# Optimization experiments

Hardware: AMD Instinct MI355X
Metric: run time of the kernel (lower is better)

The kernel has to match this reference:

```python
import jax, jax.numpy as jnp
import numpy as np

DIM = 384
HEADS = 12
WS = 7


def setup_inputs() -> dict:
    key = jax.random.key(0)
    ks = jax.random.split(key, 5)
    B, H, W = 16, 56, 56
    x = jax.random.normal(ks[0], (B, H * W, DIM), dtype=jnp.float32)
    # torch Linear weight (out,in) used as x @ W here, qkv_bias=False
    w_qkv = jax.random.normal(ks[1], (DIM, 3 * DIM), dtype=jnp.float32) * 0.02
    w_proj = jax.random.normal(ks[2], (DIM, DIM), dtype=jnp.float32) * 0.02
    b_proj = jax.random.normal(ks[3], (DIM,), dtype=jnp.float32) * 0.02
    # depthwise 3x3 conv (groups=dim): HWIO kernel (3,3,1,DIM), bias=True
    w_conv = jax.random.normal(ks[4], (3, 3, 1, DIM), dtype=jnp.float32) * 0.02
    b_conv = jnp.zeros((DIM,), jnp.float32)
    return {"x": x, "w_qkv": w_qkv, "w_proj": w_proj, "b_proj": b_proj,
            "w_conv": w_conv, "b_conv": b_conv, "H": H, "W": W}


def reference(x, w_qkv, w_proj, b_proj, w_conv, b_conv, H, W):
    B, N, C = x.shape
    hd = C // HEADS
    scale = hd ** (-0.5)
    hg, wg = H // WS, W // WS  # H,W chosen divisible by ws (no-pad fast path)

    qkv = x @ w_qkv  # (B, N, 3C)
    q, k, v = jnp.split(qkv, 3, axis=-1)

    def to_win(t):
        # (B,N,C) -> (B, n_windows, heads, ws*ws, head_dim)
        t = t.reshape(B, hg, WS, wg, WS, HEADS, hd)
        return t.transpose(0, 1, 3, 5, 2, 4, 6).reshape(B, hg * wg, HEADS, WS * WS, hd)

    qw, kw, vw = to_win(q), to_win(k), to_win(v)

    attn = jax.nn.softmax(jnp.einsum('bwhqd,bwhkd->bwhqk', qw, kw) * scale, axis=-1)
    out = jnp.einsum('bwhqk,bwhkd->bwhqd', attn, vw)
    # merge windows back: (B,nw,heads,q,d) -> (B,N,C)
    out = out.reshape(B, hg, wg, HEADS, WS, WS, hd)
    out = out.transpose(0, 1, 4, 2, 5, 3, 6).reshape(B, N, C)

    # LIM: win2img(img2win(v)) is just v as (B,C,H,W); depthwise 3x3 conv
    v_img = v.reshape(B, H, W, C).transpose(0, 3, 1, 2)
    v_lim = jax.lax.conv_general_dilated(
        v_img, w_conv, window_strides=(1, 1), padding='SAME',
        dimension_numbers=('NCHW', 'HWIO', 'NCHW'), feature_group_count=C)
    v_lim = v_lim + b_conv[None, :, None, None]
    v_lim = v_lim.reshape(B, C, N).transpose(0, 2, 1)  # (B, N, C)

    out = out + v_lim
    return out @ w_proj + b_proj
```

## Files before the change

### kernel.cpp

```cpp
#include <hip/hip_runtime.h>
#include <cstdint>
#include <cstddef>

typedef __bf16 bf16x8 __attribute__((ext_vector_type(8)));
typedef float floatx4 __attribute__((ext_vector_type(4)));

#define DEV static __device__ __forceinline__

DEV float bf2f(uint16_t u) {
    union { uint32_t i; float f; } x; x.i = ((uint32_t)u) << 16; return x.f;
}
DEV uint16_t f2bf(float f) {
    uint32_t u = __float_as_uint(f);
    uint32_t r = (u + 0x7FFFu + ((u >> 16) & 1u)) >> 16;
    return (uint16_t)r;
}
DEV bf16x8 as_bf8(uint4 u) {
    union { uint4 u; bf16x8 b; } c; c.u = u; return c.b;
}
DEV void g2l16(const void* g, void* l) {
    __builtin_amdgcn_global_load_lds(
        (const __attribute__((address_space(1))) void*)g,
        (__attribute__((address_space(3))) void*)l, 16, 0, 0);
}

union U16x8 { uint16_t h[8]; uint4 u; };

constexpr int DIMC  = 384;
constexpr int HEADS = 12;
constexpr int IMH   = 56, IMW = 56;
constexpr int NTOK  = IMH * IMW;
constexpr int BATCH = 16;
constexpr int MTOT  = BATCH * NTOK;
constexpr int QKVLD = 3 * DIMC;
constexpr int GK    = 384;
constexpr int MTILES_PAD = 200;

constexpr int CVTB  = (MTOT * DIMC) / (8 * 256);
constexpr int TQKVB = (GK * QKVLD) / 256;
constexpr int TPRJB = (GK * DIMC) / 256;

__global__ __launch_bounds__(256) void prep_kernel(
    const float* __restrict__ x,      uint16_t* __restrict__ xb,
    const float* __restrict__ w_qkv,  uint16_t* __restrict__ wqkvT,
    const float* __restrict__ w_proj, uint16_t* __restrict__ wprojT)
{
    int bid = blockIdx.x;
    int t   = threadIdx.x;
    if (bid < CVTB) {
        size_t i = ((size_t)bid * 256 + t) * 8;
        float4 a = *(const float4*)(x + i);
        float4 b = *(const float4*)(x + i + 4);
        U16x8 o;
        o.h[0] = f2bf(a.x); o.h[1] = f2bf(a.y); o.h[2] = f2bf(a.z); o.h[3] = f2bf(a.w);
        o.h[4] = f2bf(b.x); o.h[5] = f2bf(b.y); o.h[6] = f2bf(b.z); o.h[7] = f2bf(b.w);
        *(uint4*)(xb + i) = o.u;
    } else if (bid < CVTB + TQKVB) {
        int idx = (bid - CVTB) * 256 + t;
        int r = idx % GK, c = idx / GK;
        wqkvT[idx] = f2bf(w_qkv[(size_t)r * QKVLD + c]);
    } else {
        int idx = (bid - CVTB - TQKVB) * 256 + t;
        int r = idx % GK, c = idx / GK;
        wprojT[idx] = f2bf(w_proj[(size_t)r * DIMC + c]);
    }
}

template<bool CF32>
__global__ __launch_bounds__(512) void gemm_bt(const uint16_t* __restrict__ A,
                                               const uint16_t* __restrict__ Bt,
                                               const float* __restrict__ bias,
                                               void* __restrict__ Cptr,
                                               int N)
{
    __shared__ __align__(16) uint16_t sA[2][256 * 32];
    __shared__ __align__(16) uint16_t sB[2][128 * 32];

    const int t    = threadIdx.x;
    const int NB   = N >> 7;
    const int bid  = blockIdx.x;
    const int chunk = bid / (8 * NB);
    const int r     = bid % (8 * NB);
    const int bm    = chunk * 8 + (r & 7);
    const int bn    = r >> 3;
    const int wave = t >> 6, lane = t & 63;
    const int wm   = (wave >> 1) * 64;
    const int wn   = (wave & 1) * 64;
    const int lr   = lane & 15, quad = lane >> 4;
    const bool mvalid = (bm * 256 + 256) <= MTOT;

    const uint16_t* Ag = A  + (size_t)(bm * 256 + (t >> 2)) * GK + (t & 3) * 8;
    const uint16_t* Bg = Bt + (size_t)(bn * 128 + (t >> 2)) * GK + (t & 3) * 8;

    auto stage = [&](int buf, int k0) {
        g2l16(Ag + k0, sA[buf] + wave * 512);
        g2l16(Ag + (size_t)128 * GK + k0, sA[buf] + 4096 + wave * 512);
        g2l16(Bg + k0, sB[buf] + wave * 512);
    };

    floatx4 acc[4][4] = {};

    stage(0, 0);
    __syncthreads();

    #pragma unroll
    for (int ks = 0; ks < 12; ++ks) {
        const int cur = ks & 1;
        if (ks < 11) stage(cur ^ 1, (ks + 1) * 32);

        bf16x8 af[4], bfr[4];
        #pragma unroll
        for (int mt = 0; mt < 4; ++mt)
            af[mt] = *(const bf16x8*)&sA[cur][(wm + mt * 16 + lr) * 32 + quad * 8];
        #pragma unroll
        for (int nt = 0; nt < 4; ++nt)
            bfr[nt] = *(const bf16x8*)&sB[cur][(wn + nt * 16 + lr) * 32 + quad * 8];
        #pragma unroll
        for (int mt = 0; mt < 4; ++mt)
            #pragma unroll
            for (int nt = 0; nt < 4; ++nt)
                acc[mt][nt] = __builtin_amdgcn_mfma_f32_16x16x32_bf16(
                    af[mt], bfr[nt], acc[mt][nt], 0, 0, 0);

        __syncthreads();
    }

    if (!mvalid) return;

    #pragma unroll
    for (int mt = 0; mt < 4; ++mt) {
        #pragma unroll
        for (int nt = 0; nt < 4; ++nt) {
            int gc = bn * 128 + wn + nt * 16 + lr;
            float bv = bias ? bias[gc] : 0.0f;
            int gr0 = bm * 256 + wm + mt * 16 + quad * 4;
            #pragma unroll
            for (int i = 0; i < 4; ++i) {
                if constexpr (CF32) {
                    ((float*)Cptr)[(size_t)(gr0 + i) * N + gc] = acc[mt][nt][i] + bv;
                } else {
                    ((uint16_t*)Cptr)[(size_t)(gr0 + i) * N + gc] = f2bf(acc[mt][nt][i] + bv);
                }
            }
        }
    }
}

constexpr int PLD = 72;
constexpr int WAVE_ELEMS = 32 * PLD + 81 * 32;

__global__ __launch_bounds__(128) void attn_mfma(const uint16_t* __restrict__ qkv,
                                                 const float* __restrict__ wconv,
                                                 const float* __restrict__ bconv,
                                                 uint16_t* __restrict__ y)
{
    __shared__ uint16_t lds[2][WAVE_ELEMS];
    __shared__ float    warr_all[2][320];

    const int wave = threadIdx.x >> 6;
    const int lane = threadIdx.x & 63;
    const int unit = blockIdx.x * 2 + wave;
    const int h  = unit % HEADS;
    const int w  = (unit / HEADS) & 63;
    const int b  = unit / (HEADS * 64);
    const int wy = w >> 3, wx = w & 7;
    const int lr = lane & 15, quad = lane >> 4;

    uint16_t* Vt    = lds[wave];
    uint16_t* Vhalo = lds[wave] + 32 * PLD;
    float*    warr  = warr_all[wave];

    #pragma unroll
    for (int it = 0; it < 5; ++it) {
        int idx = it * 64 + lane;
        if (idx < 288) warr[idx] = wconv[(idx >> 5) * DIMC + h * 32 + (idx & 31)];
    }
    if (lane < 32) warr[288 + lane] = bconv[h * 32 + lane];

    #pragma unroll
    for (int it = 0; it < 6; ++it) {
        int u = it * 16 + (lane >> 2);
        int g = lane & 3;
        if (u < 81) {
            int hy = u / 9, hx = u % 9;
            int iy = wy * 7 + hy - 1, ix = wx * 7 + hx - 1;
            uint4 val{0, 0, 0, 0};
            if (iy >= 0 && iy < IMH && ix >= 0 && ix < IMW)
                val = *(const uint4*)(qkv + (size_t)(b * NTOK + iy * IMW + ix) * QKVLD
                                      + 2 * DIMC + h * 32 + g * 8);
            *(uint4*)&Vhalo[u * 32 + g * 8] = val;
        }
    }

    auto rowbase = [&](int i, int which) -> const uint16_t* {
        int py = i / 7, px = i % 7;
        int n = (wy * 7 + py) * IMW + wx * 7 + px;
        return qkv + (size_t)(b * NTOK + n) * QKVLD + which * DIMC + h * 32;
    };

    uint4 qf[4], kf[4];
    #pragma unroll
    for (int tm = 0; tm < 4; ++tm) {
        int i = tm * 16 + lr;
        if (i < 49) {
            qf[tm] = *(const uint4*)(rowbase(i, 0) + quad * 8);
            kf[tm] = *(const uint4*)(rowbase(i, 1) + quad * 8);
        } else {
            qf[tm] = uint4{0, 0, 0, 0};
            kf[tm] = uint4{0, 0, 0, 0};
        }
    }

    {
        int j = lane;
        if (j < 49) {
            int hrow = (j / 7 + 1) * 9 + (j % 7 + 1);
            #pragma unroll
            for (int p = 0; p < 4; ++p) {
                U16x8 tmp; tmp.u = *(const uint4*)&Vhalo[hrow * 32 + p * 8];
                #pragma unroll
                for (int q = 0; q < 8; ++q) Vt[(p * 8 + q) * PLD + j] = tmp.h[q];
            }
        } else {
            #pragma unroll
            for (int d = 0; d < 32; ++d) Vt[d * PLD + j] = 0;
        }
    }

    floatx4 S[4][4] = {};
    #pragma unroll
    for (int ta = 0; ta < 4; ++ta)
        #pragma unroll
        for (int tb = 0; tb < 4; ++tb)
            S[ta][tb] = __builtin_amdgcn_mfma_f32_16x16x32_bf16(
                as_bf8(kf[ta]), as_bf8(qf[tb]), S[ta][tb], 0, 0, 0);

    const float scale = 0.17677669529663687f;
    float psum[4] = {0.f, 0.f, 0.f, 0.f};
    #pragma unroll
    for (int ta = 0; ta < 4; ++ta) {
        #pragma unroll
        for (int tb = 0; tb < 4; ++tb) {
            #pragma unroll
            for (int i = 0; i < 4; ++i) {
                float e;
                if (ta < 3) e = __expf(S[ta][tb][i] * scale);
                else        e = (quad == 0 && i == 0)
                                ? __expf(S[ta][tb][i] * scale) : 0.0f;
                S[ta][tb][i] = e;
                psum[tb] += e;
            }
        }
    }
    #pragma unroll
    for (int tb = 0; tb < 4; ++tb) {
        float s = psum[tb];
        s += __shfl_xor(s, 16);
        s += __shfl_xor(s, 32);
        psum[tb] = 1.0f / s;
    }

    uint32_t pkv[4][4][2];
    #pragma unroll
    for (int ta = 0; ta < 4; ++ta) {
        #pragma unroll
        for (int tb = 0; tb < 4; ++tb) {
            #pragma unroll
            for (int hh = 0; hh < 2; ++hh) {
                float lo = S[ta][tb][2 * hh]     * psum[tb];
                float hi = S[ta][tb][2 * hh + 1] * psum[tb];
                asm("v_cvt_pk_bf16_f32 %0, %1, %2"
                    : "=v"(pkv[ta][tb][hh]) : "v"(lo), "v"(hi));
            }
        }
    }

    const int lo_lane = (quad & 1) * 32 + lr;
    const bool hiq = quad >= 2;
    floatx4 Ot[2][4] = {};
    #pragma unroll
    for (int kk = 0; kk < 2; ++kk) {
        uint4 pfr[4];
        #pragma unroll
        for (int tb = 0; tb < 4; ++tb) {
            uint32_t a0 = (uint32_t)__shfl((int)pkv[kk * 2][tb][0],     lo_lane);
            uint32_t b0 = (uint32_t)__shfl((int)pkv[kk * 2 + 1][tb][0], lo_lane);
            uint32_t a1 = (uint32_t)__shfl((int)pkv[kk * 2][tb][1],     lo_lane);
            uint32_t b1 = (uint32_t)__shfl((int)pkv[kk * 2 + 1][tb][1], lo_lane);
            uint32_t a2 = (uint32_t)__shfl((int)pkv[kk * 2][tb][0],     lo_lane + 16);
            uint32_t b2 = (uint32_t)__shfl((int)pkv[kk * 2 + 1][tb][0], lo_lane + 16);
            uint32_t a3 = (uint32_t)__shfl((int)pkv[kk * 2][tb][1],     lo_lane + 16);
            uint32_t b3 = (uint32_t)__shfl((int)pkv[kk * 2 + 1][tb][1], lo_lane + 16);
            pfr[tb] = uint4{hiq ? b0 : a0, hiq ? b1 : a1,
                            hiq ? b2 : a2, hiq ? b3 : a3};
        }
        bf16x8 vf[2];
        #pragma unroll
        for (int td = 0; td < 2; ++td)
            vf[td] = *(const bf16x8*)&Vt[(td * 16 + lr) * PLD + kk * 32 + quad * 8];
        #pragma unroll
        for (int td = 0; td < 2; ++td)
            #pragma unroll
            for (int tb = 0; tb < 4; ++tb)
                Ot[td][tb] = __builtin_amdgcn_mfma_f32_16x16x32_bf16(
                    vf[td], as_bf8(pfr[tb]), Ot[td][tb], 0, 0, 0);
    }

    uint16_t* convb = Vt;
    #pragma unroll
    for (int it = 0; it < 4; ++it) {
        int u = it * 64 + lane;
        if (u < 196) {
            int j = u >> 2, g = u & 3;
            int py = j / 7, px = j % 7;
            float acc[8];
            {
                float4 b0 = *(const float4*)(warr + 288 + g * 8);
                float4 b1 = *(const float4*)(warr + 288 + g * 8 + 4);
                acc[0] = b0.x; acc[1] = b0.y; acc[2] = b0.z; acc[3] = b0.w;
                acc[4] = b1.x; acc[5] = b1.y; acc[6] = b1.z; acc[7] = b1.w;
            }
            #pragma unroll
            for (int ky = 0; ky < 3; ++ky) {
                #pragma unroll
                for (int kx = 0; kx < 3; ++kx) {
                    int hrow = (py + ky) * 9 + (px + kx);
                    U16x8 v; v.u = *(const uint4*)&Vhalo[hrow * 32 + g * 8];
                    const float* wp = warr + (ky * 3 + kx) * 32 + g * 8;
                    float4 w0 = *(const float4*)wp;
                    float4 w1 = *(const float4*)(wp + 4);
                    acc[0] += bf2f(v.h[0]) * w0.x;
                    acc[1] += bf2f(v.h[1]) * w0.y;
                    acc[2] += bf2f(v.h[2]) * w0.z;
                    acc[3] += bf2f(v.h[3]) * w0.w;
                    acc[4] += bf2f(v.h[4]) * w1.x;
                    acc[5] += bf2f(v.h[5]) * w1.y;
                    acc[6] += bf2f(v.h[6]) * w1.z;
                    acc[7] += bf2f(v.h[7]) * w1.w;
                }
            }
            U16x8 rr;
            #pragma unroll
            for (int q = 0; q < 8; ++q) rr.h[q] = f2bf(acc[q]);
            *(uint4*)&convb[j * 32 + g * 8] = rr.u;
        }
    }

    #pragma unroll
    for (int tb = 0; tb < 4; ++tb) {
        int q = tb * 16 + lr;
        if (q < 49) {
            int py = q / 7, px = q % 7;
            int n = (wy * 7 + py) * IMW + wx * 7 + px;
            uint16_t* dst = y + (size_t)(b * NTOK + n) * DIMC + h * 32;
            #pragma unroll
            for (int td = 0; td < 2; ++td) {
                int d0 = td * 16 + quad * 4;
                uint2 cv = *(const uint2*)&convb[q * 32 + d0];
                float o0 = Ot[td][tb][0] + bf2f((uint16_t)(cv.x & 0xffffu));
                float o1 = Ot[td][tb][1] + bf2f((uint16_t)(cv.x >> 16));
                float o2 = Ot[td][tb][2] + bf2f((uint16_t)(cv.y & 0xffffu));
                float o3 = Ot[td][tb][3] + bf2f((uint16_t)(cv.y >> 16));
                uint32_t w0, w1;
                asm("v_cvt_pk_bf16_f32 %0, %1, %2" : "=v"(w0) : "v"(o0), "v"(o1));
                asm("v_cvt_pk_bf16_f32 %0, %1, %2" : "=v"(w1) : "v"(o2), "v"(o3));
                *(uint2*)(dst + d0) = uint2{w0, w1};
            }
        }
    }
}

extern "C" void kernel_launch(void* const* d_in, const int* in_sizes, int n_in,
                              void* d_out, int out_size, void* d_ws, size_t ws_size,
                              hipStream_t stream)
{
    const float* x      = (const float*)d_in[0];
    const float* w_qkv  = (const float*)d_in[1];
    const float* w_proj = (const float*)d_in[2];
    const float* b_proj = (const float*)d_in[3];
    const float* w_conv = (const float*)d_in[4];
    const float* b_conv = (const float*)d_in[5];
    float* out = (float*)d_out;

    char* ws = (char*)d_ws;
    uint16_t* qkv    = (uint16_t*)ws;
    uint16_t* xb     = (uint16_t*)(ws + 115605504);
    uint16_t* yb     = xb;
    uint16_t* wqkvT  = (uint16_t*)(ws + 115605504 + 38535168);
    uint16_t* wprojT = wqkvT + QKVLD * GK;

    prep_kernel<<<dim3(CVTB + TQKVB + TPRJB), 256, 0, stream>>>(
        x, xb, w_qkv, wqkvT, w_proj, wprojT);

    gemm_bt<false><<<dim3(MTILES_PAD * (QKVLD / 128)), 512, 0, stream>>>(
        xb, wqkvT, nullptr, qkv, QKVLD);

    attn_mfma<<<dim3(BATCH * 64 * HEADS / 2), 128, 0, stream>>>(
        qkv, w_conv, b_conv, yb);

    gemm_bt<true><<<dim3(MTILES_PAD * (DIMC / 128)), 512, 0, stream>>>(
        yb, wprojT, b_proj, out, DIMC);
}
```

Before: 300.9 us.

## Shrink GEMM tiles to 128x128 and use triple-buffered LDS pipeline

The bf16 GEMMs now use 128x128 tiles with 256 threads instead of 256x128 with 512 threads. This removes the padded M-tiles and the wasted tail work. The K loop is fully unrolled with a three-stage LDS ring: it prefetches two steps ahead and uses explicit vmcnt waits plus a single barrier per step, so global loads overlap MFMA work. The trade-off is more blocks and more total B-operand traffic, and correctness now depends on the hand-counted vmcnt values.

```diff
diff --git a/kernel.cpp b/kernel.cpp
--- a/kernel.cpp
+++ b/kernel.cpp
@@ -34,7 +34,6 @@
 constexpr int MTOT  = BATCH * NTOK;
 constexpr int QKVLD = 3 * DIMC;
 constexpr int GK    = 384;
-constexpr int MTILES_PAD = 200;
 
 constexpr int CVTB  = (MTOT * DIMC) / (8 * 256);
 constexpr int TQKVB = (GK * QKVLD) / 256;
@@ -67,14 +66,14 @@
 }
 
 template<bool CF32>
-__global__ __launch_bounds__(512) void gemm_bt(const uint16_t* __restrict__ A,
+__global__ __launch_bounds__(256) void gemm_bt(const uint16_t* __restrict__ A,
                                                const uint16_t* __restrict__ Bt,
                                                const float* __restrict__ bias,
                                                void* __restrict__ Cptr,
                                                int N)
 {
-    __shared__ __align__(16) uint16_t sA[2][256 * 32];
-    __shared__ __align__(16) uint16_t sB[2][128 * 32];
+    __shared__ __align__(16) uint16_t sA[3][128 * 32];
+    __shared__ __align__(16) uint16_t sB[3][128 * 32];
 
     const int t    = threadIdx.x;
     const int NB   = N >> 7;
@@ -84,48 +83,67 @@
     const int bm    = chunk * 8 + (r & 7);
     const int bn    = r >> 3;
     const int wave = t >> 6, lane = t & 63;
-    const int wm   = (wave >> 1) * 64;
-    const int wn   = (wave & 1) * 64;
+    const int wm   = (wave >> 1) * 64, wn = (wave & 1) * 64;
     const int lr   = lane & 15, quad = lane >> 4;
-    const bool mvalid = (bm * 256 + 256) <= MTOT;
-
-    const uint16_t* Ag = A  + (size_t)(bm * 256 + (t >> 2)) * GK + (t & 3) * 8;
+
+    const uint16_t* Ag = A  + (size_t)(bm * 128 + (t >> 2)) * GK + (t & 3) * 8;
     const uint16_t* Bg = Bt + (size_t)(bn * 128 + (t >> 2)) * GK + (t & 3) * 8;
 
     auto stage = [&](int buf, int k0) {
         g2l16(Ag + k0, sA[buf] + wave * 512);
-        g2l16(Ag + (size_t)128 * GK + k0, sA[buf] + 4096 + wave * 512);
+        g2l16(Ag + (size_t)64 * GK + k0, sA[buf] + 2048 + wave * 512);
         g2l16(Bg + k0, sB[buf] + wave * 512);
+        g2l16(Bg + (size_t)64 * GK + k0, sB[buf] + 2048 + wave * 512);
     };
 
     floatx4 acc[4][4] = {};
 
-    stage(0, 0);
-    __syncthreads();
-
-    #pragma unroll
-    for (int ks = 0; ks < 12; ++ks) {
-        const int cur = ks & 1;
-        if (ks < 11) stage(cur ^ 1, (ks + 1) * 32);
-
+    auto compute = [&](int buf) {
         bf16x8 af[4], bfr[4];
         #pragma unroll
         for (int mt = 0; mt < 4; ++mt)
-            af[mt] = *(const bf16x8*)&sA[cur][(wm + mt * 16 + lr) * 32 + quad * 8];
+            af[mt] = *(const bf16x8*)&sA[buf][(wm + mt * 16 + lr) * 32 + quad * 8];
         #pragma unroll
         for (int nt = 0; nt < 4; ++nt)
-            bfr[nt] = *(const bf16x8*)&sB[cur][(wn + nt * 16 + lr) * 32 + quad * 8];
+            bfr[nt] = *(const bf16x8*)&sB[buf][(wn + nt * 16 + lr) * 32 + quad * 8];
         #pragma unroll
         for (int mt = 0; mt < 4; ++mt)
             #pragma unroll
             for (int nt = 0; nt < 4; ++nt)
                 acc[mt][nt] = __builtin_amdgcn_mfma_f32_16x16x32_bf16(
                     af[mt], bfr[nt], acc[mt][nt], 0, 0, 0);
-
-        __syncthreads();
-    }
-
-    if (!mvalid) return;
+    };
+
+    stage(0, 0);
+    stage(1, 32);
+    asm volatile("s_waitcnt vmcnt(4)" ::: "memory");
+    __builtin_amdgcn_sched_barrier(0);
+    __builtin_amdgcn_s_barrier();
+    __builtin_amdgcn_sched_barrier(0);
+
+#define K_STEP(K, DOPRE, VM)                                   \
+    {                                                          \
+        if (DOPRE) stage((K + 2) % 3, (K + 2) * 32);           \
+        compute(K % 3);                                        \
+        asm volatile("s_waitcnt vmcnt(" VM ")" ::: "memory");  \
+        __builtin_amdgcn_sched_barrier(0);                     \
+        __builtin_amdgcn_s_barrier();                          \
+        __builtin_amdgcn_sched_barrier(0);                     \
+    }
+
+    K_STEP(0, 1, "4")
+    K_STEP(1, 1, "4")
+    K_STEP(2, 1, "4")
+    K_STEP(3, 1, "4")
+    K_STEP(4, 1, "4")
+    K_STEP(5, 1, "4")
+    K_STEP(6, 1, "4")
+    K_STEP(7, 1, "4")
+    K_STEP(8, 1, "4")
+    K_STEP(9, 1, "4")
+    K_STEP(10, 0, "0")
+    compute(11 % 3);
+#undef K_STEP
 
     #pragma unroll
     for (int mt = 0; mt < 4; ++mt) {
@@ -133,7 +151,7 @@
         for (int nt = 0; nt < 4; ++nt) {
             int gc = bn * 128 + wn + nt * 16 + lr;
             float bv = bias ? bias[gc] : 0.0f;
-            int gr0 = bm * 256 + wm + mt * 16 + quad * 4;
+            int gr0 = bm * 128 + wm + mt * 16 + quad * 4;
             #pragma unroll
             for (int i = 0; i < 4; ++i) {
                 if constexpr (CF32) {
@@ -392,12 +410,12 @@
     prep_kernel<<<dim3(CVTB + TQKVB + TPRJB), 256, 0, stream>>>(
         x, xb, w_qkv, wqkvT, w_proj, wprojT);
 
-    gemm_bt<false><<<dim3(MTILES_PAD * (QKVLD / 128)), 512, 0, stream>>>(
+    gemm_bt<false><<<dim3((MTOT / 128) * (QKVLD / 128)), 256, 0, stream>>>(
         xb, wqkvT, nullptr, qkv, QKVLD);
 
     attn_mfma<<<dim3(BATCH * 64 * HEADS / 2), 128, 0, stream>>>(
         qkv, w_conv, b_conv, yb);
 
-    gemm_bt<true><<<dim3(MTILES_PAD * (DIMC / 128)), 512, 0, stream>>>(
+    gemm_bt<true><<<dim3((MTOT / 128) * (DIMC / 128)), 256, 0, stream>>>(
         yb, wprojT, b_proj, out, DIMC);
 }
```

Result: no change. 297.7 us (-1.1%).
